# Kernel tuning notes

Hardware: AMD Instinct MI355X
Metric: run time of the kernel (lower is better)

Reference implementation:

```python
import jax, jax.numpy as jnp
import numpy as np

N, E, S = 50000, 800000, 3          # nodes, edges, message-passing steps
ND, ED, GD = 7, 4, 2                # raw node/edge/global feature dims
H, L = 64, 64                       # hidden and latent sizes


def _mlp3(x, W0, b0, W1, b1, W2, b2):
    # MLP([H, H, L]) with gelu between layers, none after last (dropout off).
    x = jax.nn.gelu(x @ W0 + b0)
    x = jax.nn.gelu(x @ W1 + b1)
    return x @ W2 + b2


def _ln(x, scale, bias, eps=1e-6):
    mu = jnp.mean(x, axis=-1, keepdims=True)
    xc = x - mu
    var = jnp.mean(xc * xc, axis=-1, keepdims=True)
    return xc * jax.lax.rsqrt(var + eps) * scale + bias


def setup_inputs() -> dict:
    key = jax.random.key(0)
    ks = iter(jax.random.split(key, 40))

    def W(i, o, stacked=False):
        shape = (S, i, o) if stacked else (i, o)
        return (jax.random.normal(next(ks), shape, jnp.float32) / np.sqrt(i)).astype(jnp.float32)

    inp = {
        "nodes": jax.random.normal(next(ks), (N, ND), jnp.float32),
        "edges": jax.random.normal(next(ks), (E, ED), jnp.float32),
        "glob": jax.random.normal(next(ks), (1, GD), jnp.float32),
        # node embedder MLP [H,H,L]
        "emb_n_W0": W(ND, H), "emb_n_b0": jnp.zeros((H,), jnp.float32),
        "emb_n_W1": W(H, H), "emb_n_b1": jnp.zeros((H,), jnp.float32),
        "emb_n_W2": W(H, L), "emb_n_b2": jnp.zeros((L,), jnp.float32),
        # edge embedder MLP
        "emb_e_W0": W(ED, H), "emb_e_b0": jnp.zeros((H,), jnp.float32),
        "emb_e_W1": W(H, H), "emb_e_b1": jnp.zeros((H,), jnp.float32),
        "emb_e_W2": W(H, L), "emb_e_b2": jnp.zeros((L,), jnp.float32),
        # per-step edge update MLP: in = edges(L)+senders(L)+receivers(L)+glob(GD)
        "edge_W0": W(3 * L + GD, H, True), "edge_b0": jnp.zeros((S, H), jnp.float32),
        "edge_W1": W(H, H, True), "edge_b1": jnp.zeros((S, H), jnp.float32),
        "edge_W2": W(H, L, True), "edge_b2": jnp.zeros((S, L), jnp.float32),
        # per-step node update MLP: in = nodes(L)+received(L)+glob(GD)
        "node_W0": W(2 * L + GD, H, True), "node_b0": jnp.zeros((S, H), jnp.float32),
        "node_W1": W(H, H, True), "node_b1": jnp.zeros((S, H), jnp.float32),
        "node_W2": W(H, L, True), "node_b2": jnp.zeros((S, L), jnp.float32),
        # per-step LayerNorms for nodes and edges
        "ln_n_scale": jnp.ones((S, L), jnp.float32), "ln_n_bias": jnp.zeros((S, L), jnp.float32),
        "ln_e_scale": jnp.ones((S, L), jnp.float32), "ln_e_bias": jnp.zeros((S, L), jnp.float32),
        # decoder MLP [H,H,3]
        "dec_W0": W(L, H), "dec_b0": jnp.zeros((H,), jnp.float32),
        "dec_W1": W(H, H), "dec_b1": jnp.zeros((H,), jnp.float32),
        "dec_W2": W(H, 3), "dec_b2": jnp.zeros((3,), jnp.float32),
        "senders": jax.random.randint(next(ks), (E,), 0, N),
        "receivers": jax.random.randint(next(ks), (E,), 0, N),
    }
    return inp


def reference(nodes, edges, glob,
              emb_n_W0, emb_n_b0, emb_n_W1, emb_n_b1, emb_n_W2, emb_n_b2,
              emb_e_W0, emb_e_b0, emb_e_W1, emb_e_b1, emb_e_W2, emb_e_b2,
              edge_W0, edge_b0, edge_W1, edge_b1, edge_W2, edge_b2,
              node_W0, node_b0, node_W1, node_b1, node_W2, node_b2,
              ln_n_scale, ln_n_bias, ln_e_scale, ln_e_bias,
              dec_W0, dec_b0, dec_W1, dec_b1, dec_W2, dec_b2,
              senders, receivers):
    # GraphMapFeatures embedder
    n = _mlp3(nodes, emb_n_W0, emb_n_b0, emb_n_W1, emb_n_b1, emb_n_W2, emb_n_b2)  # [N, L]
    e = _mlp3(edges, emb_e_W0, emb_e_b0, emb_e_W1, emb_e_b1, emb_e_W2, emb_e_b2)  # [E, L]
    n_nodes, n_edges = n.shape[0], e.shape[0]
    ge = jnp.broadcast_to(glob, (n_edges, glob.shape[1]))  # globals per edge (single graph)
    gn = jnp.broadcast_to(glob, (n_nodes, glob.shape[1]))  # globals per node
    steps = edge_W0.shape[0]
    for s in range(steps):
        # edge update: gather sender/receiver node feats, concat, MLP
        e_in = jnp.concatenate([e, n[senders], n[receivers], ge], axis=1)  # [E, 3L+GD]
        new_e = _mlp3(e_in, edge_W0[s], edge_b0[s], edge_W1[s], edge_b1[s], edge_W2[s], edge_b2[s])
        # scatter-aggregate to receivers (jraph default: segment_sum)
        recv = jax.ops.segment_sum(new_e, receivers, num_segments=n_nodes)  # [N, L]
        n_in = jnp.concatenate([n, recv, gn], axis=1)  # [N, 2L+GD]
        new_n = _mlp3(n_in, node_W0[s], node_b0[s], node_W1[s], node_b1[s], node_W2[s], node_b2[s])
        # residual skip connections then per-step LayerNorm
        n = _ln(n + new_n, ln_n_scale[s], ln_n_bias[s])
        e = _ln(e + new_e, ln_e_scale[s], ln_e_bias[s])
    # decoder on nodes -> [N, 3]
    return _mlp3(n, dec_W0, dec_b0, dec_W1, dec_b1, dec_W2, dec_b2)
```

## Files before the change

kernel.cpp:

```cpp
#include <hip/hip_runtime.h>

#define N_NODES 50000
#define N_EDGES 800000
#define NSTEPS 3
#define NBLK_SCAN 196

typedef __attribute__((ext_vector_type(8))) short bf16x8;
typedef __attribute__((ext_vector_type(4))) float f32x4;


__device__ __forceinline__ float ldf(const void* p, long i, int bf) {
    if (bf) {
        unsigned int u = ((const unsigned short*)p)[i];
        u <<= 16;
        return __uint_as_float(u);
    }
    return ((const float*)p)[i];
}

__device__ __forceinline__ unsigned short f2bf(float f) {
    return (unsigned short)((__float_as_uint(f) + 0x8000u) >> 16);
}

__device__ __forceinline__ float bf2f(unsigned short u) {
    return __uint_as_float(((unsigned int)u) << 16);
}

__device__ __forceinline__ unsigned int cvtpk(float a, float b) {
    unsigned int r;
    asm("v_cvt_pk_bf16_f32 %0, %1, %2" : "=v"(r) : "v"(a), "v"(b));
    return r;
}

__device__ __forceinline__ float gelu_f(float x) {
    float x2 = x * x;
    float m = x * fmaf(-0.10294325f, x2, -2.30220847f);
    float e = __builtin_amdgcn_exp2f(m);
    return x * __builtin_amdgcn_rcpf(1.0f + e);
}

__device__ __forceinline__ void zero4(f32x4 a[4]) {
#pragma unroll
    for (int t = 0; t < 4; t++) a[t] = (f32x4){0.f, 0.f, 0.f, 0.f};
}

__device__ __forceinline__ void mfma_chunk(f32x4 acc[4], bf16x8 a, const unsigned short* bb) {
    acc[0] = __builtin_amdgcn_mfma_f32_16x16x32_bf16(a, *(const bf16x8*)(bb + 0), acc[0], 0, 0, 0);
    acc[1] = __builtin_amdgcn_mfma_f32_16x16x32_bf16(a, *(const bf16x8*)(bb + 512), acc[1], 0, 0, 0);
    acc[2] = __builtin_amdgcn_mfma_f32_16x16x32_bf16(a, *(const bf16x8*)(bb + 1024), acc[2], 0, 0, 0);
    acc[3] = __builtin_amdgcn_mfma_f32_16x16x32_bf16(a, *(const bf16x8*)(bb + 1536), acc[3], 0, 0, 0);
}

__global__ void detect_kernel(const void* probe, int* flag) {
    if (threadIdx.x == 0 && blockIdx.x == 0) {
        unsigned int w = *(const unsigned int*)probe;
        *flag = (w == 0x3F803F80u) ? 1 : 0;
    }
}

__global__ void hist_kernel(const int* __restrict__ receivers, int* __restrict__ counts) {
    int i = blockIdx.x * 256 + threadIdx.x;
    if (i < N_EDGES) atomicAdd(&counts[receivers[i]], 1);
}

__global__ void scan_partial(const int* __restrict__ counts, int* __restrict__ base,
                             int* __restrict__ blockSums) {
    __shared__ int sm[256];
    int b = blockIdx.x, t = threadIdx.x, i = b * 256 + t;
    int v = (i < N_NODES) ? counts[i] : 0;
    sm[t] = v;
    __syncthreads();
    for (int off = 1; off < 256; off <<= 1) {
        int x = (t >= off) ? sm[t - off] : 0;
        __syncthreads();
        sm[t] += x;
        __syncthreads();
    }
    if (i < N_NODES) base[i] = sm[t] - v;
    if (t == 255) blockSums[b] = sm[255];
}

__global__ void scan_tops(int* __restrict__ blockSums, int* __restrict__ tops) {
    __shared__ int sm[256];
    int t = threadIdx.x;
    int v = (t < NBLK_SCAN) ? blockSums[t] : 0;
    sm[t] = v;
    __syncthreads();
    for (int off = 1; off < 256; off <<= 1) {
        int x = (t >= off) ? sm[t - off] : 0;
        __syncthreads();
        sm[t] += x;
        __syncthreads();
    }
    if (t < NBLK_SCAN) tops[t] = sm[t] - v;
}

__global__ void scan_add(int* __restrict__ base, const int* __restrict__ tops,
                         int* __restrict__ cursor) {
    int b = blockIdx.x, i = b * 256 + threadIdx.x;
    if (i < N_NODES) {
        int v = base[i] + tops[b];
        base[i] = v;
        cursor[i] = v;
    }
}

__global__ void scatter_kernel(const int* __restrict__ senders,
                               const int* __restrict__ receivers, int* __restrict__ cursor,
                               int* __restrict__ ss, int* __restrict__ rsrt,
                               int* __restrict__ perm) {
    int i = blockIdx.x * 256 + threadIdx.x;
    if (i < N_EDGES) {
        int r = receivers[i];
        int pos = atomicAdd(&cursor[r], 1);
        ss[pos] = senders[i];
        rsrt[pos] = r;
        perm[pos] = i;
    }
}

struct PrepPtrs {
    const void* W[14];
    const void* eb0;
    const void* nb0;
    const void* glob;
};

#define PREP_WTOTAL 139264
__global__ void prep_all(PrepPtrs p, unsigned short* WbBase, float* b0eff_e, float* b0eff_n,
                         const int* __restrict__ flagp) {
    const int totals[14] = {36864, 12288, 12288, 24576, 12288, 12288, 2048,
                            4096,  4096,  2048,  4096,  4096,  4096,  4096};
    const int ksrc[14] = {192, 64, 64, 128, 64, 64, 7, 64, 64, 4, 64, 64, 64, 64};
    const int sstride[14] = {12416, 4096, 4096, 8320, 4096, 4096, 448,
                             4096,  4096, 256,  4096, 4096, 4096, 4096};
    const int nch[14] = {6, 2, 2, 4, 2, 2, 1, 2, 2, 1, 2, 2, 2, 2};
    const int rowperm[14] = {0, 1, 1, 0, 1, 1, 0, 1, 1, 0, 1, 1, 1, 1};

    const int bf = *flagp;
    int i = blockIdx.x * 256 + threadIdx.x;
    if (i < PREP_WTOTAL) {
        int e = 0, base = 0;
        while (i >= base + totals[e]) { base += totals[e]; e++; }
        int il = i - base;
        int j = il & 7, lane = (il >> 3) & 63, t = (il >> 9) & 3;
        int c = (il >> 11) % nch[e], s = il / (2048 * nch[e]);
        int k = c * 32 + (lane >> 4) * 8 + j;
        int col = t * 16 + (lane & 15);
        int ks = k;
        if (rowperm[e] || (e == 0 && k < 64)) ks = ((k & 3) << 4) | (k >> 2);
        WbBase[i] = (k < ksrc[e]) ? f2bf(ldf(p.W[e], (long)s * sstride[e] + (long)ks * 64 + col, bf))
                                  : (unsigned short)0;
    } else if (i < PREP_WTOTAL + 384) {
        int i2 = i - PREP_WTOTAL;
        float g0 = ldf(p.glob, 0, bf), g1 = ldf(p.glob, 1, bf);
        if (i2 < 192) {
            int s = i2 >> 6, col = i2 & 63;
            b0eff_e[i2] = ldf(p.eb0, i2, bf) + g0 * ldf(p.W[0], (long)s * 12416 + 192 * 64 + col, bf)
                                             + g1 * ldf(p.W[0], (long)s * 12416 + 193 * 64 + col, bf);
        } else {
            int il = i2 - 192;
            int s = il >> 6, col = il & 63;
            b0eff_n[il] = ldf(p.nb0, il, bf) + g0 * ldf(p.W[3], (long)s * 8320 + 128 * 64 + col, bf)
                                             + g1 * ldf(p.W[3], (long)s * 8320 + 129 * 64 + col, bf);
        }
    }
}

template <int DIN, int OUT_BF>
__global__ __launch_bounds__(256) void embed_mfma(
    const void* __restrict__ xin, const unsigned short* __restrict__ Wb0, const void* b0,
    const unsigned short* __restrict__ Wb1, const void* b1,
    const unsigned short* __restrict__ Wb2, const void* b2, void* __restrict__ outp,
    unsigned short* __restrict__ out_bf, const int* __restrict__ perm, int R,
    const int* __restrict__ flagp) {
    __shared__ __align__(16) unsigned short Xs[64 * 40];
    __shared__ __align__(16) unsigned short hbuf[64 * 72];
    const int bf = *flagp;
    const int tid = threadIdx.x;
    const long rb = (long)blockIdx.x * 64;
    const int lane = tid & 63, w = tid >> 6, q = lane >> 4, l15 = lane & 15;
    const int arow = 16 * w + l15, aoff = q * 8;
    unsigned short* hw = hbuf + w * 16 * 72;

    {
        int r = tid >> 2, seg = tid & 3;
        long idx = rb + r;
        long src = (perm != nullptr && idx < R) ? (long)perm[idx] : idx;
        unsigned short u[8];
#pragma unroll
        for (int j = 0; j < 8; j++) {
            int col = seg * 8 + j;
            u[j] = (col < DIN && idx < R) ? f2bf(ldf(xin, src * DIN + col, bf)) : (unsigned short)0;
        }
        *(uint4*)&Xs[r * 40 + seg * 8] = *(uint4*)u;
    }

    f32x4 acc[4];
    zero4(acc);
    {
        bf16x8 a = *(const bf16x8*)&Xs[arow * 40 + aoff];
        mfma_chunk(acc, a, Wb0 + lane * 8);
        float bb[4];
#pragma unroll
        for (int t = 0; t < 4; t++) bb[t] = ldf(b0, t * 16 + l15, bf);
#pragma unroll
        for (int reg = 0; reg < 4; reg++) {
            uint2 v;
            v.x = cvtpk(gelu_f(acc[0][reg] + bb[0]), gelu_f(acc[1][reg] + bb[1]));
            v.y = cvtpk(gelu_f(acc[2][reg] + bb[2]), gelu_f(acc[3][reg] + bb[3]));
            *(uint2*)&hw[(q * 4 + reg) * 72 + l15 * 4] = v;
        }
    }
    zero4(acc);
    {
#pragma unroll
        for (int c = 0; c < 2; c++) {
            bf16x8 a = *(const bf16x8*)&hw[l15 * 72 + c * 32 + aoff];
            mfma_chunk(acc, a, Wb1 + c * 2048 + lane * 8);
        }
        float bb[4];
#pragma unroll
        for (int t = 0; t < 4; t++) bb[t] = ldf(b1, t * 16 + l15, bf);
#pragma unroll
        for (int reg = 0; reg < 4; reg++) {
            uint2 v;
            v.x = cvtpk(gelu_f(acc[0][reg] + bb[0]), gelu_f(acc[1][reg] + bb[1]));
            v.y = cvtpk(gelu_f(acc[2][reg] + bb[2]), gelu_f(acc[3][reg] + bb[3]));
            *(uint2*)&hw[(q * 4 + reg) * 72 + l15 * 4] = v;
        }
    }
    zero4(acc);
    {
#pragma unroll
        for (int c = 0; c < 2; c++) {
            bf16x8 a = *(const bf16x8*)&hw[l15 * 72 + c * 32 + aoff];
            mfma_chunk(acc, a, Wb2 + c * 2048 + lane * 8);
        }
    }
    if (OUT_BF) {
#pragma unroll
        for (int t = 0; t < 4; t++) {
            int col = t * 16 + l15;
            float b = ldf(b2, col, bf);
#pragma unroll
            for (int reg = 0; reg < 4; reg++)
                hw[(q * 4 + reg) * 72 + col] = f2bf(acc[t][reg] + b);
        }
#pragma unroll
        for (int p = 0; p < 2; p++) {
            int r = 16 * w + p * 8 + (lane >> 3), o = lane & 7;
            long idx = rb + r;
            if (idx < R)
                *(uint4*)&((unsigned short*)outp)[idx * 64 + o * 8] =
                    *(const uint4*)&hbuf[r * 72 + o * 8];
        }
    } else {
#pragma unroll
        for (int t = 0; t < 4; t++) {
            int col = t * 16 + l15;
            float b = ldf(b2, col, bf);
#pragma unroll
            for (int reg = 0; reg < 4; reg++) {
                long idx = rb + 16 * w + q * 4 + reg;
                if (idx < R) {
                    float v = acc[t][reg] + b;
                    ((float*)outp)[idx * 64 + col] = v;
                    out_bf[idx * 64 + col] = f2bf(v);
                }
            }
        }
    }
}

#define EST 72
#define NST 68
template <int S0, int LAST>
__global__ __launch_bounds__(256) void edge_step(
    unsigned short* __restrict__ e_lat, const unsigned short* __restrict__ n_bf,
    const int* __restrict__ ss, const int* __restrict__ rsrt, const int* __restrict__ perm,
    const void* __restrict__ xe_raw, const unsigned short* __restrict__ We0, const void* eb0_,
    const unsigned short* __restrict__ We1, const void* eb1_,
    const unsigned short* __restrict__ We2, const void* eb2_,
    const unsigned short* __restrict__ Wb0, const unsigned short* __restrict__ Wb1,
    const unsigned short* __restrict__ Wb2, const float* __restrict__ b0eff, const void* b1,
    const void* b2, const void* lnsc, const void* lnbi, float* __restrict__ recvbuf, int s,
    const int* __restrict__ flagp) {
    __shared__ __align__(16) unsigned short Ee[64 * EST];
    __shared__ __align__(16) unsigned short NsNr[128 * NST];
    __shared__ int rcvs[64];
    float* newe = (float*)NsNr;

    const int bf = *flagp;
    const int tid = threadIdx.x;
    const long rb = (long)blockIdx.x * 64;
    const int lane = tid & 63, w = tid >> 6, q = lane >> 4, l15 = lane & 15;
    const int arow = 16 * w + l15, aoff = q * 8;
    unsigned short* hw = Ee + w * 16 * EST;

#pragma unroll
    for (int p = 0; p < 2; p++) {
        int r = 16 * w + p * 8 + (lane >> 3), o = lane & 7;
        long node = ss[rb + r];
        *(uint4*)&NsNr[r * NST + o * 8] = ((const uint4*)(n_bf + node * 64))[o];
    }
#pragma unroll
    for (int p = 0; p < 2; p++) {
        int r = 16 * w + p * 8 + (lane >> 3), o = lane & 7;
        long node = rsrt[rb + r];
        *(uint4*)&NsNr[(64 + r) * NST + o * 8] = ((const uint4*)(n_bf + node * 64))[o];
    }
    if (lane < 16) rcvs[16 * w + lane] = rsrt[rb + 16 * w + lane];

    float ein[4][4];
    f32x4 acc[4];

    if (S0) {
        zero4(acc);
        {
            bf16x8 a = (bf16x8){0, 0, 0, 0, 0, 0, 0, 0};
            if (q == 0) {
                long src = perm[rb + arow];
                unsigned short u[8] = {0, 0, 0, 0, 0, 0, 0, 0};
#pragma unroll
                for (int j = 0; j < 4; j++) u[j] = f2bf(ldf(xe_raw, src * 4 + j, bf));
                a = *(const bf16x8*)u;
            }
            mfma_chunk(acc, a, We0 + lane * 8);
            float bb[4];
#pragma unroll
            for (int t = 0; t < 4; t++) bb[t] = ldf(eb0_, t * 16 + l15, bf);
#pragma unroll
            for (int reg = 0; reg < 4; reg++) {
                uint2 v;
                v.x = cvtpk(gelu_f(acc[0][reg] + bb[0]), gelu_f(acc[1][reg] + bb[1]));
                v.y = cvtpk(gelu_f(acc[2][reg] + bb[2]), gelu_f(acc[3][reg] + bb[3]));
                *(uint2*)&hw[(q * 4 + reg) * EST + l15 * 4] = v;
            }
        }
        zero4(acc);
        {
#pragma unroll
            for (int c = 0; c < 2; c++) {
                bf16x8 a = *(const bf16x8*)&hw[l15 * EST + c * 32 + aoff];
                mfma_chunk(acc, a, We1 + c * 2048 + lane * 8);
            }
            float bb[4];
#pragma unroll
            for (int t = 0; t < 4; t++) bb[t] = ldf(eb1_, t * 16 + l15, bf);
#pragma unroll
            for (int reg = 0; reg < 4; reg++) {
                uint2 v;
                v.x = cvtpk(gelu_f(acc[0][reg] + bb[0]), gelu_f(acc[1][reg] + bb[1]));
                v.y = cvtpk(gelu_f(acc[2][reg] + bb[2]), gelu_f(acc[3][reg] + bb[3]));
                *(uint2*)&hw[(q * 4 + reg) * EST + l15 * 4] = v;
            }
        }
        zero4(acc);
        {
#pragma unroll
            for (int c = 0; c < 2; c++) {
                bf16x8 a = *(const bf16x8*)&hw[l15 * EST + c * 32 + aoff];
                mfma_chunk(acc, a, We2 + c * 2048 + lane * 8);
            }
            float bb[4];
#pragma unroll
            for (int t = 0; t < 4; t++) bb[t] = ldf(eb2_, t * 16 + l15, bf);
#pragma unroll
            for (int reg = 0; reg < 4; reg++) {
                float e0 = acc[0][reg] + bb[0], e1 = acc[1][reg] + bb[1];
                float e2 = acc[2][reg] + bb[2], e3 = acc[3][reg] + bb[3];
                ein[reg][0] = e0; ein[reg][1] = e1; ein[reg][2] = e2; ein[reg][3] = e3;
                uint2 v;
                v.x = cvtpk(e0, e1);
                v.y = cvtpk(e2, e3);
                *(uint2*)&Ee[(16 * w + q * 4 + reg) * EST + l15 * 4] = v;
            }
        }
    } else {
#pragma unroll
        for (int p = 0; p < 2; p++) {
            int r = 16 * w + p * 8 + (lane >> 3), o = lane & 7;
            *(uint4*)&Ee[r * EST + o * 8] = ((const uint4*)(e_lat + (rb + r) * 64))[o];
        }
        if (!LAST) {
#pragma unroll
            for (int reg = 0; reg < 4; reg++) {
                uint2 pv = *(const uint2*)&Ee[(16 * w + q * 4 + reg) * EST + l15 * 4];
                ein[reg][0] = __uint_as_float(pv.x << 16);
                ein[reg][1] = __uint_as_float(pv.x & 0xffff0000u);
                ein[reg][2] = __uint_as_float(pv.y << 16);
                ein[reg][3] = __uint_as_float(pv.y & 0xffff0000u);
            }
        }
    }

    zero4(acc);
    {
        const unsigned short* B = Wb0 + (long)s * 6 * 2048 + lane * 8;
#pragma unroll
        for (int c = 0; c < 2; c++) {
            bf16x8 a = *(const bf16x8*)&Ee[arow * EST + c * 32 + aoff];
            mfma_chunk(acc, a, B + c * 2048);
        }
#pragma unroll
        for (int c = 0; c < 2; c++) {
            bf16x8 a = *(const bf16x8*)&NsNr[arow * NST + c * 32 + aoff];
            mfma_chunk(acc, a, B + (2 + c) * 2048);
        }
#pragma unroll
        for (int c = 0; c < 2; c++) {
            bf16x8 a = *(const bf16x8*)&NsNr[(64 + arow) * NST + c * 32 + aoff];
            mfma_chunk(acc, a, B + (4 + c) * 2048);
        }
        float bb[4];
#pragma unroll
        for (int t = 0; t < 4; t++) bb[t] = b0eff[s * 64 + t * 16 + l15];
#pragma unroll
        for (int reg = 0; reg < 4; reg++) {
            uint2 v;
            v.x = cvtpk(gelu_f(acc[0][reg] + bb[0]), gelu_f(acc[1][reg] + bb[1]));
            v.y = cvtpk(gelu_f(acc[2][reg] + bb[2]), gelu_f(acc[3][reg] + bb[3]));
            *(uint2*)&hw[(q * 4 + reg) * EST + l15 * 4] = v;
        }
    }
    zero4(acc);
    {
        const unsigned short* B = Wb1 + (long)s * 2 * 2048 + lane * 8;
#pragma unroll
        for (int c = 0; c < 2; c++) {
            bf16x8 a = *(const bf16x8*)&hw[l15 * EST + c * 32 + aoff];
            mfma_chunk(acc, a, B + c * 2048);
        }
        float bb[4];
#pragma unroll
        for (int t = 0; t < 4; t++) bb[t] = ldf(b1, (long)s * 64 + t * 16 + l15, bf);
#pragma unroll
        for (int reg = 0; reg < 4; reg++) {
            uint2 v;
            v.x = cvtpk(gelu_f(acc[0][reg] + bb[0]), gelu_f(acc[1][reg] + bb[1]));
            v.y = cvtpk(gelu_f(acc[2][reg] + bb[2]), gelu_f(acc[3][reg] + bb[3]));
            *(uint2*)&hw[(q * 4 + reg) * EST + l15 * 4] = v;
        }
    }
    zero4(acc);
    {
        const unsigned short* B = Wb2 + (long)s * 2 * 2048 + lane * 8;
#pragma unroll
        for (int c = 0; c < 2; c++) {
            bf16x8 a = *(const bf16x8*)&hw[l15 * EST + c * 32 + aoff];
            mfma_chunk(acc, a, B + c * 2048);
        }
    }
    __syncthreads();

    float fin[4][4];
#pragma unroll
    for (int t = 0; t < 4; t++) {
        const float b = ldf(b2, (long)s * 64 + t * 16 + l15, bf);
#pragma unroll
        for (int reg = 0; reg < 4; reg++) fin[reg][t] = acc[t][reg] + b;
    }
    float lsc[4], lbi[4];
    if (!LAST) {
#pragma unroll
        for (int t = 0; t < 4; t++) {
            lsc[t] = ldf(lnsc, (long)s * 64 + t * 16 + l15, bf);
            lbi[t] = ldf(lnbi, (long)s * 64 + t * 16 + l15, bf);
        }
    }
#pragma unroll
    for (int reg = 0; reg < 4; reg++) {
        const int lr = q * 4 + reg;
#pragma unroll
        for (int t = 0; t < 4; t++) newe[w * 1056 + lr * 66 + t * 16 + l15] = fin[reg][t];
        if (!LAST) {
            float u[4], ssum = 0.f;
#pragma unroll
            for (int t = 0; t < 4; t++) {
                u[t] = ein[reg][t] + fin[reg][t];
                ssum += u[t];
            }
#pragma unroll
            for (int m = 1; m < 16; m <<= 1) ssum += __shfl_xor(ssum, m, 64);
            const float mu = ssum * (1.0f / 64.0f);
            float d[4], vv = 0.f;
#pragma unroll
            for (int t = 0; t < 4; t++) { d[t] = u[t] - mu; vv += d[t] * d[t]; }
#pragma unroll
            for (int m = 1; m < 16; m <<= 1) vv += __shfl_xor(vv, m, 64);
            const float rs = rsqrtf(vv * (1.0f / 64.0f) + 1e-6f);
            uint2 v;
            v.x = cvtpk(d[0] * rs * lsc[0] + lbi[0], d[1] * rs * lsc[1] + lbi[1]);
            v.y = cvtpk(d[2] * rs * lsc[2] + lbi[2], d[3] * rs * lsc[3] + lbi[3]);
            *(uint2*)&Ee[(16 * w + lr) * EST + l15 * 4] = v;
        }
    }

    if (!LAST) {
#pragma unroll
        for (int p = 0; p < 2; p++) {
            int r = 16 * w + p * 8 + (lane >> 3), o = lane & 7;
            *(uint4*)&e_lat[(rb + r) * 64 + o * 8] = *(const uint4*)&Ee[r * EST + o * 8];
        }
    }
    {
        const int col = tid & 63, g = tid >> 6;
        float a = 0.f;
#pragma unroll
        for (int rr = 0; rr < 16; rr++) {
            const int r = 16 * g + rr;
            a += newe[g * 1056 + rr * 66 + col];
            if (rr == 15 || rcvs[r + 1] != rcvs[r]) {
                atomicAdd(&recvbuf[(long)rcvs[r] * 64 + col], a);
                a = 0.f;
            }
        }
    }
}

#define NXS 136
template <int FINAL>
__global__ __launch_bounds__(256) void node_update_mfma(
    float* __restrict__ n_lat, unsigned short* __restrict__ n_bf, float* __restrict__ recvbuf,
    const unsigned short* __restrict__ Wb0, const float* __restrict__ b0eff,
    const unsigned short* __restrict__ Wb1, const void* b1,
    const unsigned short* __restrict__ Wb2, const void* b2, const void* lnsc,
    const void* lnbi, const unsigned short* __restrict__ WbD0, const void* db0,
    const unsigned short* __restrict__ WbD1, const void* db1, const void* dW2,
    const void* db2, void* __restrict__ outp, int s, const int* __restrict__ flagp) {
    __shared__ __align__(16) unsigned short Xs[64 * NXS];
    __shared__ __align__(16) unsigned short hbuf[64 * 72];
    const int bf = *flagp;
    const int tid = threadIdx.x;
    const long rb = (long)blockIdx.x * 64;
    const int lane = tid & 63, w = tid >> 6, q = lane >> 4, l15 = lane & 15;
    const int arow = 16 * w + l15, aoff = q * 8;
    unsigned short* hw = hbuf + w * 16 * 72;

#pragma unroll
    for (int p = 0; p < 2; p++) {
        int r = 16 * w + p * 8 + (lane >> 3), o = lane & 7;
        long idx = rb + r;
        uint4 v = {0u, 0u, 0u, 0u};
        if (idx < N_NODES) v = ((const uint4*)(n_bf + idx * 64))[o];
        *(uint4*)&Xs[r * NXS + o * 8] = v;
    }
#pragma unroll
    for (int p = 0; p < 2; p++) {
        int r = 16 * w + p * 8 + (lane >> 3), o = lane & 7;
        long idx = rb + r;
        uint4 v = {0u, 0u, 0u, 0u};
        if (idx < N_NODES) {
            const float* src = recvbuf + idx * 64 + o * 8;
            float4 x0 = *(const float4*)src, x1 = *(const float4*)(src + 4);
            v.x = cvtpk(x0.x, x0.y);
            v.y = cvtpk(x0.z, x0.w);
            v.z = cvtpk(x1.x, x1.y);
            v.w = cvtpk(x1.z, x1.w);
        }
        *(uint4*)&Xs[r * NXS + 64 + o * 8] = v;
    }

    f32x4 acc[4];
    zero4(acc);
    {
        const unsigned short* B = Wb0 + (long)s * 4 * 2048 + lane * 8;
#pragma unroll
        for (int c = 0; c < 4; c++) {
            bf16x8 a = *(const bf16x8*)&Xs[arow * NXS + c * 32 + aoff];
            mfma_chunk(acc, a, B + c * 2048);
        }
        float bb[4];
#pragma unroll
        for (int t = 0; t < 4; t++) bb[t] = b0eff[s * 64 + t * 16 + l15];
#pragma unroll
        for (int reg = 0; reg < 4; reg++) {
            uint2 v;
            v.x = cvtpk(gelu_f(acc[0][reg] + bb[0]), gelu_f(acc[1][reg] + bb[1]));
            v.y = cvtpk(gelu_f(acc[2][reg] + bb[2]), gelu_f(acc[3][reg] + bb[3]));
            *(uint2*)&hw[(q * 4 + reg) * 72 + l15 * 4] = v;
        }
    }
    zero4(acc);
    {
        const unsigned short* B = Wb1 + (long)s * 2 * 2048 + lane * 8;
#pragma unroll
        for (int c = 0; c < 2; c++) {
            bf16x8 a = *(const bf16x8*)&hw[l15 * 72 + c * 32 + aoff];
            mfma_chunk(acc, a, B + c * 2048);
        }
        float bb[4];
#pragma unroll
        for (int t = 0; t < 4; t++) bb[t] = ldf(b1, (long)s * 64 + t * 16 + l15, bf);
#pragma unroll
        for (int reg = 0; reg < 4; reg++) {
            uint2 v;
            v.x = cvtpk(gelu_f(acc[0][reg] + bb[0]), gelu_f(acc[1][reg] + bb[1]));
            v.y = cvtpk(gelu_f(acc[2][reg] + bb[2]), gelu_f(acc[3][reg] + bb[3]));
            *(uint2*)&hw[(q * 4 + reg) * 72 + l15 * 4] = v;
        }
    }
    zero4(acc);
    {
        const unsigned short* B = Wb2 + (long)s * 2 * 2048 + lane * 8;
#pragma unroll
        for (int c = 0; c < 2; c++) {
            bf16x8 a = *(const bf16x8*)&hw[l15 * 72 + c * 32 + aoff];
            mfma_chunk(acc, a, B + c * 2048);
        }
    }
    float b2v[4], lsc[4], lbi[4];
#pragma unroll
    for (int t = 0; t < 4; t++) {
        b2v[t] = ldf(b2, (long)s * 64 + t * 16 + l15, bf);
        lsc[t] = ldf(lnsc, (long)s * 64 + t * 16 + l15, bf);
        lbi[t] = ldf(lnbi, (long)s * 64 + t * 16 + l15, bf);
    }
#pragma unroll
    for (int reg = 0; reg < 4; reg++) {
        const int rowl = 16 * w + q * 4 + reg;
        const long idx = rb + rowl;
        const bool valid = idx < N_NODES;
        float u[4], ssum = 0.f;
#pragma unroll
        for (int t = 0; t < 4; t++) {
            const int col = t * 16 + l15;
            float xn = valid ? n_lat[idx * 64 + col] : 0.f;
            u[t] = xn + acc[t][reg] + b2v[t];
            ssum += u[t];
        }
#pragma unroll
        for (int m = 1; m < 16; m <<= 1) ssum += __shfl_xor(ssum, m, 64);
        const float mu = ssum * (1.0f / 64.0f);
        float d[4], vv = 0.f;
#pragma unroll
        for (int t = 0; t < 4; t++) { d[t] = u[t] - mu; vv += d[t] * d[t]; }
#pragma unroll
        for (int m = 1; m < 16; m <<= 1) vv += __shfl_xor(vv, m, 64);
        const float rs = rsqrtf(vv * (1.0f / 64.0f) + 1e-6f);
        if (FINAL) {
            uint2 v;
            v.x = cvtpk(d[0] * rs * lsc[0] + lbi[0], d[1] * rs * lsc[1] + lbi[1]);
            v.y = cvtpk(d[2] * rs * lsc[2] + lbi[2], d[3] * rs * lsc[3] + lbi[3]);
            *(uint2*)&hw[(q * 4 + reg) * 72 + l15 * 4] = v;
        } else if (valid) {
#pragma unroll
            for (int t = 0; t < 4; t++) {
                const int col = t * 16 + l15;
                float v = d[t] * rs * lsc[t] + lbi[t];
                n_lat[idx * 64 + col] = v;
                n_bf[idx * 64 + col] = f2bf(v);
                recvbuf[idx * 64 + col] = 0.f;
            }
        }
    }
    if (FINAL) {
        zero4(acc);
        {
#pragma unroll
            for (int c = 0; c < 2; c++) {
                bf16x8 a = *(const bf16x8*)&hw[l15 * 72 + c * 32 + aoff];
                mfma_chunk(acc, a, WbD0 + c * 2048 + lane * 8);
            }
            float bb[4];
#pragma unroll
            for (int t = 0; t < 4; t++) bb[t] = ldf(db0, t * 16 + l15, bf);
#pragma unroll
            for (int reg = 0; reg < 4; reg++) {
                uint2 v;
                v.x = cvtpk(gelu_f(acc[0][reg] + bb[0]), gelu_f(acc[1][reg] + bb[1]));
                v.y = cvtpk(gelu_f(acc[2][reg] + bb[2]), gelu_f(acc[3][reg] + bb[3]));
                *(uint2*)&hw[(q * 4 + reg) * 72 + l15 * 4] = v;
            }
        }
        zero4(acc);
        {
#pragma unroll
            for (int c = 0; c < 2; c++) {
                bf16x8 a = *(const bf16x8*)&hw[l15 * 72 + c * 32 + aoff];
                mfma_chunk(acc, a, WbD1 + c * 2048 + lane * 8);
            }
            float bb[4];
#pragma unroll
            for (int t = 0; t < 4; t++) bb[t] = ldf(db1, t * 16 + l15, bf);
#pragma unroll
            for (int reg = 0; reg < 4; reg++) {
                uint2 v;
                v.x = cvtpk(gelu_f(acc[0][reg] + bb[0]), gelu_f(acc[1][reg] + bb[1]));
                v.y = cvtpk(gelu_f(acc[2][reg] + bb[2]), gelu_f(acc[3][reg] + bb[3]));
                *(uint2*)&hw[(q * 4 + reg) * 72 + l15 * 4] = v;
            }
        }
        const int col = tid & 63;
        const int r0 = w * 16;
        if (col < 3) {
            float a[16];
            const float b = ldf(db2, col, bf);
#pragma unroll
            for (int i = 0; i < 16; i++) a[i] = b;
            for (int k = 0; k < 64; k++) {
                const int ksrc2 = ((k & 3) << 4) | (k >> 2);
                float wv = ldf(dW2, (long)ksrc2 * 3 + col, bf);
#pragma unroll
                for (int i = 0; i < 16; i++) a[i] = fmaf(bf2f(hw[i * 72 + k]), wv, a[i]);
            }
            for (int i = 0; i < 16; i++) {
                const long idx = rb + r0 + i;
                if (idx < N_NODES) {
                    if (bf)
                        ((unsigned short*)outp)[idx * 3 + col] = f2bf(a[i]);
                    else
                        ((float*)outp)[idx * 3 + col] = a[i];
                }
            }
        }
    }
}

extern "C" void kernel_launch(void* const* d_in, const int* in_sizes, int n_in, void* d_out,
                              int out_size, void* d_ws, size_t ws_size, hipStream_t stream) {
    const void* nodes = d_in[0];
    const void* edges = d_in[1];
    const void* glob = d_in[2];
    const void *enW0 = d_in[3], *enb0 = d_in[4], *enW1 = d_in[5], *enb1 = d_in[6],
               *enW2 = d_in[7], *enb2 = d_in[8];
    const void *eeW0 = d_in[9], *eeb0 = d_in[10], *eeW1 = d_in[11], *eeb1 = d_in[12],
               *eeW2 = d_in[13], *eeb2 = d_in[14];
    const void *eW0 = d_in[15], *eb0 = d_in[16], *eW1 = d_in[17], *eb1 = d_in[18],
               *eW2 = d_in[19], *eb2 = d_in[20];
    const void *nW0 = d_in[21], *nb0 = d_in[22], *nW1 = d_in[23], *nb1 = d_in[24],
               *nW2 = d_in[25], *nb2 = d_in[26];
    const void *lnns = d_in[27], *lnnb = d_in[28], *lnes = d_in[29], *lneb = d_in[30];
    const void *dW0 = d_in[31], *db0 = d_in[32], *dW1 = d_in[33], *db1 = d_in[34],
               *dW2 = d_in[35], *db2 = d_in[36];
    const int* senders = (const int*)d_in[37];
    const int* receivers = (const int*)d_in[38];

    float* n_lat = (float*)d_ws;
    float* recvb = n_lat + 3200000;
    float* b0eff_e = recvb + 3200000;
    float* b0eff_n = b0eff_e + 192;
    int* flag = (int*)(b0eff_n + 192);
    unsigned short* e_lat = (unsigned short*)(b0eff_n + 256);
    unsigned short* n_bf = e_lat + 51200000;
    unsigned short* WbBase = n_bf + 3200000;
    unsigned short* WbE0 = WbBase;
    unsigned short* WbE1 = WbBase + 36864;
    unsigned short* WbE2 = WbBase + 49152;
    unsigned short* WbN0 = WbBase + 61440;
    unsigned short* WbN1 = WbBase + 86016;
    unsigned short* WbN2 = WbBase + 98304;
    unsigned short* WbNE0 = WbBase + 110592;
    unsigned short* WbNE1 = WbBase + 112640;
    unsigned short* WbNE2 = WbBase + 116736;
    unsigned short* WbEE0 = WbBase + 120832;
    unsigned short* WbEE1 = WbBase + 122880;
    unsigned short* WbEE2 = WbBase + 126976;
    unsigned short* WbD0 = WbBase + 131072;
    unsigned short* WbD1 = WbBase + 135168;
    int* counts = (int*)(WbBase + 139264 + 64);
    int* sbase = counts + N_NODES;
    int* cursor = sbase + N_NODES;
    int* blockSums = cursor + N_NODES;
    int* tops = blockSums + 256;
    int* ss = tops + 256;
    int* rsrt = ss + N_EDGES;
    int* perm = rsrt + N_EDGES;

    detect_kernel<<<1, 64, 0, stream>>>(lnns, flag);

    PrepPtrs pp;
    pp.W[0] = eW0;  pp.W[1] = eW1;  pp.W[2] = eW2;
    pp.W[3] = nW0;  pp.W[4] = nW1;  pp.W[5] = nW2;
    pp.W[6] = enW0; pp.W[7] = enW1; pp.W[8] = enW2;
    pp.W[9] = eeW0; pp.W[10] = eeW1; pp.W[11] = eeW2;
    pp.W[12] = dW0; pp.W[13] = dW1;
    pp.eb0 = eb0; pp.nb0 = nb0; pp.glob = glob;
    prep_all<<<(PREP_WTOTAL + 384 + 255) / 256, 256, 0, stream>>>(pp, WbBase, b0eff_e, b0eff_n,
                                                                  flag);
    hipMemsetAsync(recvb, 0, (size_t)N_NODES * 64 * sizeof(float), stream);
    hipMemsetAsync(counts, 0, (size_t)N_NODES * sizeof(int), stream);

    hist_kernel<<<(N_EDGES + 255) / 256, 256, 0, stream>>>(receivers, counts);
    scan_partial<<<NBLK_SCAN, 256, 0, stream>>>(counts, sbase, blockSums);
    scan_tops<<<1, 256, 0, stream>>>(blockSums, tops);
    scan_add<<<NBLK_SCAN, 256, 0, stream>>>(sbase, tops, cursor);
    scatter_kernel<<<(N_EDGES + 255) / 256, 256, 0, stream>>>(senders, receivers, cursor, ss,
                                                              rsrt, perm);

    embed_mfma<7, 0><<<(N_NODES + 63) / 64, 256, 0, stream>>>(
        nodes, WbNE0, enb0, WbNE1, enb1, WbNE2, enb2, n_lat, n_bf, (const int*)nullptr,
        N_NODES, flag);

    edge_step<1, 0><<<N_EDGES / 64, 256, 0, stream>>>(
        e_lat, n_bf, ss, rsrt, perm, edges, WbEE0, eeb0, WbEE1, eeb1, WbEE2, eeb2,
        WbE0, WbE1, WbE2, b0eff_e, eb1, eb2, lnes, lneb, recvb, 0, flag);
    node_update_mfma<0><<<(N_NODES + 63) / 64, 256, 0, stream>>>(
        n_lat, n_bf, recvb, WbN0, b0eff_n, WbN1, nb1, WbN2, nb2, lnns, lnnb,
        nullptr, nullptr, nullptr, nullptr, nullptr, nullptr, nullptr, 0, flag);

    edge_step<0, 0><<<N_EDGES / 64, 256, 0, stream>>>(
        e_lat, n_bf, ss, rsrt, perm, edges, WbEE0, eeb0, WbEE1, eeb1, WbEE2, eeb2,
        WbE0, WbE1, WbE2, b0eff_e, eb1, eb2, lnes, lneb, recvb, 1, flag);
    node_update_mfma<0><<<(N_NODES + 63) / 64, 256, 0, stream>>>(
        n_lat, n_bf, recvb, WbN0, b0eff_n, WbN1, nb1, WbN2, nb2, lnns, lnnb,
        nullptr, nullptr, nullptr, nullptr, nullptr, nullptr, nullptr, 1, flag);

    edge_step<0, 1><<<N_EDGES / 64, 256, 0, stream>>>(
        e_lat, n_bf, ss, rsrt, perm, edges, WbEE0, eeb0, WbEE1, eeb1, WbEE2, eeb2,
        WbE0, WbE1, WbE2, b0eff_e, eb1, eb2, lnes, lneb, recvb, 2, flag);
    node_update_mfma<1><<<(N_NODES + 63) / 64, 256, 0, stream>>>(
        n_lat, n_bf, recvb, WbN0, b0eff_n, WbN1, nb1, WbN2, nb2, lnns, lnnb,
        WbD0, db0, WbD1, db1, dW2, db2, d_out, 2, flag);
}
```

Before: 670.0 us.

## Permute W2 output columns so epilogues use vectorized float4 stores

Extends the k-row permutation in weight prep to every layer that feeds later MFMA stages, including the first edge/node layers. As a result each lane holds 4 contiguous output columns. The epilogues of the embed MLP, edge step and node update now write fp32/bf16 rows with float4/uint2 stores instead of scattered scalar stores. The newe LDS buffer stride is padded to 68 to fit float4 writes. It relies on the permuted column layout matching across all kernels, which is a correctness risk if any consumer expects the old ordering.

```diff
diff --git a/kernel.cpp b/kernel.cpp
--- a/kernel.cpp
+++ b/kernel.cpp
@@ -135,7 +135,7 @@
     const int sstride[14] = {12416, 4096, 4096, 8320, 4096, 4096, 448,
                              4096,  4096, 256,  4096, 4096, 4096, 4096};
     const int nch[14] = {6, 2, 2, 4, 2, 2, 1, 2, 2, 1, 2, 2, 2, 2};
-    const int rowperm[14] = {0, 1, 1, 0, 1, 1, 0, 1, 1, 0, 1, 1, 1, 1};
+    const int rowperm[14] = {1, 1, 1, 1, 1, 1, 0, 1, 1, 0, 1, 1, 1, 1};
 
     const int bf = *flagp;
     int i = blockIdx.x * 256 + threadIdx.x;
@@ -148,7 +148,10 @@
         int k = c * 32 + (lane >> 4) * 8 + j;
         int col = t * 16 + (lane & 15);
         int ks = k;
-        if (rowperm[e] || (e == 0 && k < 64)) ks = ((k & 3) << 4) | (k >> 2);
+        if (rowperm[e]) {
+            int kb = k & 63;
+            ks = (k & ~63) | (((kb & 3) << 4) | (kb >> 2));
+        }
         WbBase[i] = (k < ksrc[e]) ? f2bf(ldf(p.W[e], (long)s * sstride[e] + (long)ks * 64 + col, bf))
                                   : (unsigned short)0;
     } else if (i < PREP_WTOTAL + 384) {
@@ -238,14 +241,16 @@
             mfma_chunk(acc, a, Wb2 + c * 2048 + lane * 8);
         }
     }
+    float bb[4];
+#pragma unroll
+    for (int t = 0; t < 4; t++) bb[t] = ldf(b2, t * 16 + l15, bf);
     if (OUT_BF) {
 #pragma unroll
-        for (int t = 0; t < 4; t++) {
-            int col = t * 16 + l15;
-            float b = ldf(b2, col, bf);
-#pragma unroll
-            for (int reg = 0; reg < 4; reg++)
-                hw[(q * 4 + reg) * 72 + col] = f2bf(acc[t][reg] + b);
+        for (int reg = 0; reg < 4; reg++) {
+            uint2 v;
+            v.x = cvtpk(acc[0][reg] + bb[0], acc[1][reg] + bb[1]);
+            v.y = cvtpk(acc[2][reg] + bb[2], acc[3][reg] + bb[3]);
+            *(uint2*)&hw[(q * 4 + reg) * 72 + l15 * 4] = v;
         }
 #pragma unroll
         for (int p = 0; p < 2; p++) {
@@ -257,17 +262,16 @@
         }
     } else {
 #pragma unroll
-        for (int t = 0; t < 4; t++) {
-            int col = t * 16 + l15;
-            float b = ldf(b2, col, bf);
-#pragma unroll
-            for (int reg = 0; reg < 4; reg++) {
-                long idx = rb + 16 * w + q * 4 + reg;
-                if (idx < R) {
-                    float v = acc[t][reg] + b;
-                    ((float*)outp)[idx * 64 + col] = v;
-                    out_bf[idx * 64 + col] = f2bf(v);
-                }
+        for (int reg = 0; reg < 4; reg++) {
+            long idx = rb + 16 * w + q * 4 + reg;
+            if (idx < R) {
+                float4 v4 = make_float4(acc[0][reg] + bb[0], acc[1][reg] + bb[1],
+                                        acc[2][reg] + bb[2], acc[3][reg] + bb[3]);
+                *(float4*)&((float*)outp)[idx * 64 + l15 * 4] = v4;
+                uint2 v;
+                v.x = cvtpk(v4.x, v4.y);
+                v.y = cvtpk(v4.z, v4.w);
+                *(uint2*)&out_bf[idx * 64 + l15 * 4] = v;
             }
         }
     }
@@ -368,12 +372,11 @@
             for (int t = 0; t < 4; t++) bb[t] = ldf(eb2_, t * 16 + l15, bf);
 #pragma unroll
             for (int reg = 0; reg < 4; reg++) {
-                float e0 = acc[0][reg] + bb[0], e1 = acc[1][reg] + bb[1];
-                float e2 = acc[2][reg] + bb[2], e3 = acc[3][reg] + bb[3];
-                ein[reg][0] = e0; ein[reg][1] = e1; ein[reg][2] = e2; ein[reg][3] = e3;
+#pragma unroll
+                for (int t = 0; t < 4; t++) ein[reg][t] = acc[t][reg] + bb[t];
                 uint2 v;
-                v.x = cvtpk(e0, e1);
-                v.y = cvtpk(e2, e3);
+                v.x = cvtpk(ein[reg][0], ein[reg][1]);
+                v.y = cvtpk(ein[reg][2], ein[reg][3]);
                 *(uint2*)&Ee[(16 * w + q * 4 + reg) * EST + l15 * 4] = v;
             }
         }
@@ -455,11 +458,14 @@
     __syncthreads();
 
     float fin[4][4];
-#pragma unroll
-    for (int t = 0; t < 4; t++) {
-        const float b = ldf(b2, (long)s * 64 + t * 16 + l15, bf);
-#pragma unroll
-        for (int reg = 0; reg < 4; reg++) fin[reg][t] = acc[t][reg] + b;
+    {
+        float bb[4];
+#pragma unroll
+        for (int t = 0; t < 4; t++) bb[t] = ldf(b2, (long)s * 64 + t * 16 + l15, bf);
+#pragma unroll
+        for (int reg = 0; reg < 4; reg++)
+#pragma unroll
+            for (int t = 0; t < 4; t++) fin[reg][t] = acc[t][reg] + bb[t];
     }
     float lsc[4], lbi[4];
     if (!LAST) {
@@ -472,8 +478,8 @@
 #pragma unroll
     for (int reg = 0; reg < 4; reg++) {
         const int lr = q * 4 + reg;
-#pragma unroll
-        for (int t = 0; t < 4; t++) newe[w * 1056 + lr * 66 + t * 16 + l15] = fin[reg][t];
+        *(float4*)&newe[w * 1088 + lr * 68 + l15 * 4] =
+            make_float4(fin[reg][0], fin[reg][1], fin[reg][2], fin[reg][3]);
         if (!LAST) {
             float u[4], ssum = 0.f;
 #pragma unroll
@@ -510,7 +516,7 @@
 #pragma unroll
         for (int rr = 0; rr < 16; rr++) {
             const int r = 16 * g + rr;
-            a += newe[g * 1056 + rr * 66 + col];
+            a += newe[g * 1088 + rr * 68 + col];
             if (rr == 15 || rcvs[r + 1] != rcvs[r]) {
                 atomicAdd(&recvbuf[(long)rcvs[r] * 64 + col], a);
                 a = 0.f;
@@ -622,14 +628,15 @@
         const int rowl = 16 * w + q * 4 + reg;
         const long idx = rb + rowl;
         const bool valid = idx < N_NODES;
+        float4 xn4 = make_float4(0.f, 0.f, 0.f, 0.f);
+        if (valid) xn4 = *(const float4*)&n_lat[idx * 64 + l15 * 4];
         float u[4], ssum = 0.f;
-#pragma unroll
-        for (int t = 0; t < 4; t++) {
-            const int col = t * 16 + l15;
-            float xn = valid ? n_lat[idx * 64 + col] : 0.f;
-            u[t] = xn + acc[t][reg] + b2v[t];
-            ssum += u[t];
-        }
+        u[0] = xn4.x + acc[0][reg] + b2v[0];
+        u[1] = xn4.y + acc[1][reg] + b2v[1];
+        u[2] = xn4.z + acc[2][reg] + b2v[2];
+        u[3] = xn4.w + acc[3][reg] + b2v[3];
+#pragma unroll
+        for (int t = 0; t < 4; t++) ssum += u[t];
 #pragma unroll
         for (int m = 1; m < 16; m <<= 1) ssum += __shfl_xor(ssum, m, 64);
         const float mu = ssum * (1.0f / 64.0f);
@@ -645,14 +652,14 @@
             v.y = cvtpk(d[2] * rs * lsc[2] + lbi[2], d[3] * rs * lsc[3] + lbi[3]);
             *(uint2*)&hw[(q * 4 + reg) * 72 + l15 * 4] = v;
         } else if (valid) {
-#pragma unroll
-            for (int t = 0; t < 4; t++) {
-                const int col = t * 16 + l15;
-                float v = d[t] * rs * lsc[t] + lbi[t];
-                n_lat[idx * 64 + col] = v;
-                n_bf[idx * 64 + col] = f2bf(v);
-                recvbuf[idx * 64 + col] = 0.f;
-            }
+            float4 v4 = make_float4(d[0] * rs * lsc[0] + lbi[0], d[1] * rs * lsc[1] + lbi[1],
+                                    d[2] * rs * lsc[2] + lbi[2], d[3] * rs * lsc[3] + lbi[3]);
+            *(float4*)&n_lat[idx * 64 + l15 * 4] = v4;
+            uint2 v;
+            v.x = cvtpk(v4.x, v4.y);
+            v.y = cvtpk(v4.z, v4.w);
+            *(uint2*)&n_bf[idx * 64 + l15 * 4] = v;
+            *(float4*)&recvbuf[idx * 64 + l15 * 4] = make_float4(0.f, 0.f, 0.f, 0.f);
         }
     }
     if (FINAL) {
```

New measurement: 666.1 us (median of 2 runs). Within noise of the previous version (-0.6%).
